# Kernel tuning notes

Hardware: AMD Instinct MI355X
Metric: run time of the kernel (lower is better)

Reference implementation:

```python
import jax, jax.numpy as jnp
import numpy as np

B, N, K, D = 256, 64, 12, 128


def setup_inputs() -> dict:
    key = jax.random.key(0)
    ks = jax.random.split(key, 12)
    s = 1.0 / np.sqrt(D)
    inp = {
        "nodes_hidden": jax.random.normal(ks[0], (B, N, D), jnp.float32),
        "neighbors_hidden": jax.random.normal(ks[1], (B, N, K, D), jnp.float32),
        # binary neighbor-validity mask (float, as in the torch code)
        "mask": (jax.random.uniform(ks[2], (B, N, K)) < 0.7).astype(jnp.float32),
        "Wq": jax.random.uniform(ks[3], (D, D), jnp.float32, -s, s),
        "bq": jax.random.uniform(ks[4], (D,), jnp.float32, -s, s),
        "Wk": jax.random.uniform(ks[5], (D, D), jnp.float32, -s, s),
        "bk": jax.random.uniform(ks[6], (D,), jnp.float32, -s, s),
        "Wv": jax.random.uniform(ks[7], (D, D), jnp.float32, -s, s),
        "bv": jax.random.uniform(ks[8], (D,), jnp.float32, -s, s),
        # W_att: Linear(2D -> 1); split into the query half and key half of its weight
        "wa_q": jax.random.uniform(ks[9], (D,), jnp.float32, -s, s),
        "wa_k": jax.random.uniform(ks[10], (D,), jnp.float32, -s, s),
        "ba": jax.random.uniform(ks[11], (), jnp.float32, -s, s),
    }
    return inp


def reference(nodes_hidden, neighbors_hidden, mask, Wq, bq, Wk, bk, Wv, bv, wa_q, wa_k, ba):
    # prepend the node itself to its neighbor list: [B,N,K+1,D]
    nh = jnp.concatenate([nodes_hidden[:, :, None, :], neighbors_hidden], axis=2)
    # prepend an always-valid slot to the mask: [B,N,K+1]
    m = jnp.concatenate([jnp.ones(mask.shape[:-1] + (1,), mask.dtype), mask], axis=-1)

    q = nodes_hidden @ Wq + bq            # [B,N,D]
    k = nh @ Wk + bk                      # [B,N,K+1,D]
    v = nh @ Wv + bv                      # [B,N,K+1,D]

    # W_att(cat([q,k])) == q.wa_q + k.wa_k + ba  (avoids materializing the 2D concat)
    sim = (q @ wa_q)[:, :, None] + k @ wa_k + ba   # [B,N,K+1]
    sim = jnp.where(sim >= 0, sim, 0.2 * sim)      # LeakyReLU(0.2)
    sim = jnp.exp(sim) * m                         # masked exp (matches torch exactly)
    attn = sim / (jnp.sum(sim, axis=-1, keepdims=True) + 1e-16)
    return jnp.einsum('bnk,bnkd->bnd', attn, v)    # [B,N,D]
```

## Files before the change

### kernel.cpp

```cpp
#include <hip/hip_runtime.h>


#define B_  256
#define N_  64
#define K_  12
#define D_  128
#define BN  (B_ * N_)
#define TP    4
#define TILES 4
#define ROWS  16
#define HB_STRIDE 132

__global__ void prep_kernel(const float* __restrict__ Wq, const float* __restrict__ bq,
                            const float* __restrict__ Wk, const float* __restrict__ bk,
                            const float* __restrict__ wa_q, const float* __restrict__ wa_k,
                            float* __restrict__ ws) {
    int g = blockIdx.x;
    int l = threadIdx.x;
    const float* row;
    const float* wa;
    float* outp;
    if (g < 128)      { row = Wq + g * D_;         wa = wa_q; outp = ws + g; }
    else if (g < 256) { row = Wk + (g - 128) * D_; wa = wa_k; outp = ws + 128 + (g - 128); }
    else if (g == 256){ row = bq;                  wa = wa_q; outp = ws + 256; }
    else              { row = bk;                  wa = wa_k; outp = ws + 257; }

    float2 r = ((const float2*)row)[l];
    float2 w = ((const float2*)wa)[l];
    float p = r.x * w.x + r.y * w.y;
    #pragma unroll
    for (int m = 1; m < 64; m <<= 1) p += __shfl_xor(p, m, 64);
    if (l == 0) *outp = p;
}

__device__ __forceinline__ void gll16(const float* g, float* l) {
    __builtin_amdgcn_global_load_lds(
        (const __attribute__((address_space(1))) unsigned int*)g,
        (__attribute__((address_space(3))) unsigned int*)l, 16, 0, 0);
}

__global__ void __launch_bounds__(256)
fused_kernel(const float* __restrict__ nodes, const float* __restrict__ neigh,
             const float* __restrict__ mask, const float* __restrict__ ba_p,
             const float* __restrict__ ws, const float* __restrict__ Wv,
             const float* __restrict__ bv, float* __restrict__ out) {
    __shared__ float nb[2][TP * K_ * D_];
    __shared__ float ndb[2][TP * D_];
    __shared__ float mb[2][TP * K_];
    __shared__ float hb[ROWS * HB_STRIDE];
    __shared__ float scL[ROWS];

    const int t    = threadIdx.x;
    const int wave = t >> 6;
    const int l    = t & 63;
    const int li   = l & 31;
    const int h    = l >> 5;
    const int j8   = l & 7;

    const float cq  = ws[256];
    const float ckb = ws[257];
    const float ba  = ba_p[0];
    const float cst = cq + ckb + ba;
    const float4 wqe4 = ((const float4*)ws)[li];
    const float4 wke4 = ((const float4*)(ws + 128))[li];

    const int base_pair = blockIdx.x * ROWS;

    #define STAGE(buf, tt) do {                                               \
        const int tb_ = base_pair + (tt) * TP;                                \
        const float* ns_ = neigh + (size_t)tb_ * (K_ * D_);                   \
        _Pragma("unroll")                                                     \
        for (int i_ = 0; i_ < 6; ++i_)                                        \
            gll16(ns_ + i_ * 1024 + t * 4, &nb[buf][i_ * 1024 + t * 4]);      \
        if (wave < 2)                                                         \
            gll16(nodes + (size_t)tb_ * D_ + t * 4, &ndb[buf][t * 4]);        \
        else if (wave == 2 && l < 12)                                         \
            gll16(mask + (size_t)tb_ * K_ + l * 4, &mb[buf][l * 4]);          \
    } while (0)

    #define COMPUTE(buf, tt) do {                                             \
        const float* nbp_ = &nb[buf][wave * (K_ * D_)];                       \
        const float* ndp_ = &ndb[buf][wave * D_];                             \
        const float4 nv_ = *(const float4*)(ndp_ + 4 * li);                   \
        float4 x0_ = *(const float4*)(nbp_ + (0 + h) * D_ + 4 * li);          \
        float4 x1_ = *(const float4*)(nbp_ + (2 + h) * D_ + 4 * li);          \
        float4 x2_ = *(const float4*)(nbp_ + (4 + h) * D_ + 4 * li);          \
        float4 x3_ = *(const float4*)(nbp_ + (6 + h) * D_ + 4 * li);          \
        float4 x4_ = *(const float4*)(nbp_ + (8 + h) * D_ + 4 * li);          \
        float4 x5_ = *(const float4*)(nbp_ + (10 + h) * D_ + 4 * li);         \
        float v0 = x0_.x*wke4.x + x0_.y*wke4.y + x0_.z*wke4.z + x0_.w*wke4.w; \
        float v1 = x1_.x*wke4.x + x1_.y*wke4.y + x1_.z*wke4.z + x1_.w*wke4.w; \
        float v2 = x2_.x*wke4.x + x2_.y*wke4.y + x2_.z*wke4.z + x2_.w*wke4.w; \
        float v3 = x3_.x*wke4.x + x3_.y*wke4.y + x3_.z*wke4.z + x3_.w*wke4.w; \
        float v4 = x4_.x*wke4.x + x4_.y*wke4.y + x4_.z*wke4.z + x4_.w*wke4.w; \
        float v5 = x5_.x*wke4.x + x5_.y*wke4.y + x5_.z*wke4.z + x5_.w*wke4.w; \
        float v6 = nv_.x*wke4.x + nv_.y*wke4.y + nv_.z*wke4.z + nv_.w*wke4.w; \
        float v7 = nv_.x*wqe4.x + nv_.y*wqe4.y + nv_.z*wqe4.z + nv_.w*wqe4.w; \
        float A0, A1, A2, A3;                                                 \
        {                                                                     \
            const bool hi_ = (l & 1);                                         \
            float g0 = __shfl_xor(hi_ ? v0 : v1, 1, 64);                      \
            float g1 = __shfl_xor(hi_ ? v2 : v3, 1, 64);                      \
            float g2 = __shfl_xor(hi_ ? v4 : v5, 1, 64);                      \
            float g3 = __shfl_xor(hi_ ? v6 : v7, 1, 64);                      \
            A0 = (hi_ ? v1 : v0) + g0;                                        \
            A1 = (hi_ ? v3 : v2) + g1;                                        \
            A2 = (hi_ ? v5 : v4) + g2;                                        \
            A3 = (hi_ ? v7 : v6) + g3;                                        \
        }                                                                     \
        float B0, B1;                                                         \
        {                                                                     \
            const bool hi_ = (l & 2);                                         \
            float g0 = __shfl_xor(hi_ ? A0 : A1, 2, 64);                      \
            float g1 = __shfl_xor(hi_ ? A2 : A3, 2, 64);                      \
            B0 = (hi_ ? A1 : A0) + g0;                                        \
            B1 = (hi_ ? A3 : A2) + g1;                                        \
        }                                                                     \
        float c;                                                              \
        {                                                                     \
            const bool hi_ = (l & 4);                                         \
            float g = __shfl_xor(hi_ ? B0 : B1, 4, 64);                       \
            c = (hi_ ? B1 : B0) + g;                                          \
        }                                                                     \
        c += __shfl_xor(c, 8, 64);                                            \
        c += __shfl_xor(c, 16, 64);                                           \
        const float pq_  = __shfl(c, 7, 8);                                   \
        const float pkn_ = __shfl(c, 6, 8);                                   \
        const float base_ = pq_ + cst;                                        \
        float s0_ = base_ + pkn_;                                             \
        s0_ = (s0_ >= 0.0f) ? s0_ : 0.2f * s0_;                               \
        const float e0_ = __expf(s0_);                                        \
        float sj_ = base_ + c;                                                \
        sj_ = (sj_ >= 0.0f) ? sj_ : 0.2f * sj_;                               \
        float ej_ = 0.0f;                                                     \
        if (j8 < 6) ej_ = __expf(sj_) * mb[buf][wave * K_ + 2 * j8 + h];      \
        const float an_ = (h == 0) ? e0_ : 0.0f;                              \
        float ax = an_ * nv_.x, ay = an_ * nv_.y;                             \
        float az = an_ * nv_.z, aw = an_ * nv_.w;                             \
        float Se_ = 0.0f;                                                     \
        {                                                                     \
            float bi_;                                                        \
            bi_ = __shfl(ej_, 0, 8); Se_ += bi_;                              \
            ax += bi_*x0_.x; ay += bi_*x0_.y; az += bi_*x0_.z; aw += bi_*x0_.w; \
            bi_ = __shfl(ej_, 1, 8); Se_ += bi_;                              \
            ax += bi_*x1_.x; ay += bi_*x1_.y; az += bi_*x1_.z; aw += bi_*x1_.w; \
            bi_ = __shfl(ej_, 2, 8); Se_ += bi_;                              \
            ax += bi_*x2_.x; ay += bi_*x2_.y; az += bi_*x2_.z; aw += bi_*x2_.w; \
            bi_ = __shfl(ej_, 3, 8); Se_ += bi_;                              \
            ax += bi_*x3_.x; ay += bi_*x3_.y; az += bi_*x3_.z; aw += bi_*x3_.w; \
            bi_ = __shfl(ej_, 4, 8); Se_ += bi_;                              \
            ax += bi_*x4_.x; ay += bi_*x4_.y; az += bi_*x4_.z; aw += bi_*x4_.w; \
            bi_ = __shfl(ej_, 5, 8); Se_ += bi_;                              \
            ax += bi_*x5_.x; ay += bi_*x5_.y; az += bi_*x5_.z; aw += bi_*x5_.w; \
        }                                                                     \
        ax += __shfl_xor(ax, 32, 64);                                         \
        ay += __shfl_xor(ay, 32, 64);                                         \
        az += __shfl_xor(az, 32, 64);                                         \
        aw += __shfl_xor(aw, 32, 64);                                         \
        Se_ += __shfl_xor(Se_, 32, 64);                                       \
        const float S_   = e0_ + Se_;                                         \
        const float inv_ = 1.0f / (S_ + 1e-16f);                              \
        if (h == 0) {                                                         \
            const int lrow_ = (tt) * TP + wave;                               \
            float4 o_;                                                        \
            o_.x = ax * inv_;                                                 \
            o_.y = ay * inv_;                                                 \
            o_.z = az * inv_;                                                 \
            o_.w = aw * inv_;                                                 \
            *(float4*)(hb + lrow_ * HB_STRIDE + 4 * li) = o_;                 \
            if (li == 0) scL[lrow_] = S_ * inv_;                              \
        }                                                                     \
    } while (0)

    STAGE(0, 0);
    __syncthreads();
    #pragma unroll
    for (int tt = 0; tt < TILES; ++tt) {
        const int cur = tt & 1;
        if (tt + 1 < TILES) STAGE((tt + 1) & 1, tt + 1);
        __builtin_amdgcn_sched_barrier(0);
        COMPUTE(cur, tt);
        __syncthreads();
    }
    #undef STAGE
    #undef COMPUTE

    const int rg = t >> 5;
    const int cg = t & 31;
    const float4* wv4 = (const float4*)Wv;
    const float* hr0 = hb + rg * HB_STRIDE;
    const float* hr1 = hb + (rg + 8) * HB_STRIDE;

    float4 acc0 = make_float4(0.0f, 0.0f, 0.0f, 0.0f);
    float4 acc1 = make_float4(0.0f, 0.0f, 0.0f, 0.0f);
    #pragma unroll 8
    for (int kq = 0; kq < 32; ++kq) {
        const float4 a0 = *(const float4*)(hr0 + 4 * kq);
        const float4 a1 = *(const float4*)(hr1 + 4 * kq);
        #pragma unroll
        for (int e = 0; e < 4; ++e) {
            const float4 w = wv4[(4 * kq + e) * 32 + cg];
            const float f0 = (e == 0) ? a0.x : (e == 1) ? a0.y : (e == 2) ? a0.z : a0.w;
            const float f1 = (e == 0) ? a1.x : (e == 1) ? a1.y : (e == 2) ? a1.z : a1.w;
            acc0.x += f0 * w.x; acc0.y += f0 * w.y;
            acc0.z += f0 * w.z; acc0.w += f0 * w.w;
            acc1.x += f1 * w.x; acc1.y += f1 * w.y;
            acc1.z += f1 * w.z; acc1.w += f1 * w.w;
        }
    }

    const float4 bvv = ((const float4*)bv)[cg];
    {
        const float s = scL[rg];
        float4 o;
        o.x = acc0.x + bvv.x * s;
        o.y = acc0.y + bvv.y * s;
        o.z = acc0.z + bvv.z * s;
        o.w = acc0.w + bvv.w * s;
        *(float4*)(out + (size_t)(base_pair + rg) * D_ + cg * 4) = o;
    }
    {
        const float s = scL[rg + 8];
        float4 o;
        o.x = acc1.x + bvv.x * s;
        o.y = acc1.y + bvv.y * s;
        o.z = acc1.z + bvv.z * s;
        o.w = acc1.w + bvv.w * s;
        *(float4*)(out + (size_t)(base_pair + rg + 8) * D_ + cg * 4) = o;
    }
}

extern "C" void kernel_launch(void* const* d_in, const int* in_sizes, int n_in,
                              void* d_out, int out_size, void* d_ws, size_t ws_size,
                              hipStream_t stream) {
    const float* nodes = (const float*)d_in[0];
    const float* neigh = (const float*)d_in[1];
    const float* mask  = (const float*)d_in[2];
    const float* Wq    = (const float*)d_in[3];
    const float* bq    = (const float*)d_in[4];
    const float* Wk    = (const float*)d_in[5];
    const float* bk    = (const float*)d_in[6];
    const float* Wv    = (const float*)d_in[7];
    const float* bv    = (const float*)d_in[8];
    const float* wa_q  = (const float*)d_in[9];
    const float* wa_k  = (const float*)d_in[10];
    const float* ba    = (const float*)d_in[11];
    float* out = (float*)d_out;
    float* ws  = (float*)d_ws;

    prep_kernel<<<258, 64, 0, stream>>>(Wq, bq, Wk, bk, wa_q, wa_k, ws);
    fused_kernel<<<BN / ROWS, 256, 0, stream>>>(nodes, neigh, mask, ba, ws, Wv, bv, out);
}
```

Before: 191.6 us.

## Give each wave private LDS slabs with vmcnt-based pipelining instead of block barriers

Each wave now stages and processes its own four consecutive node rows in two private LDS slots. It waits on its own outstanding global-to-LDS loads with s_waitcnt vmcnt rather than a block-wide __syncthreads per tile. Mask values are loaded straight into registers up front instead of being staged through LDS. This removes barrier stalls between waves and lets each wave overlap its next load with its current compute. In exchange, correctness now depends on hand-counted vmcnt values and on the in-order completion of these loads.

```diff
diff --git a/kernel.cpp b/kernel.cpp
--- a/kernel.cpp
+++ b/kernel.cpp
@@ -6,10 +6,9 @@
 #define K_  12
 #define D_  128
 #define BN  (B_ * N_)
-#define TP    4
-#define TILES 4
-#define ROWS  16
+#define ROWS 16
 #define HB_STRIDE 132
+#define SLOT_F 1664
 
 __global__ void prep_kernel(const float* __restrict__ Wq, const float* __restrict__ bq,
                             const float* __restrict__ Wk, const float* __restrict__ bk,
@@ -44,9 +43,7 @@
              const float* __restrict__ mask, const float* __restrict__ ba_p,
              const float* __restrict__ ws, const float* __restrict__ Wv,
              const float* __restrict__ bv, float* __restrict__ out) {
-    __shared__ float nb[2][TP * K_ * D_];
-    __shared__ float ndb[2][TP * D_];
-    __shared__ float mb[2][TP * K_];
+    __shared__ float slab[8][SLOT_F];
     __shared__ float hb[ROWS * HB_STRIDE];
     __shared__ float scL[ROWS];
 
@@ -65,29 +62,33 @@
     const float4 wke4 = ((const float4*)(ws + 128))[li];
 
     const int base_pair = blockIdx.x * ROWS;
-
-    #define STAGE(buf, tt) do {                                               \
-        const int tb_ = base_pair + (tt) * TP;                                \
-        const float* ns_ = neigh + (size_t)tb_ * (K_ * D_);                   \
+    const int idx0 = base_pair + wave * 4;
+
+    float mv0 = (j8 < 6) ? mask[(size_t)(idx0 + 0) * K_ + 2 * j8 + h] : 0.0f;
+    float mv1 = (j8 < 6) ? mask[(size_t)(idx0 + 1) * K_ + 2 * j8 + h] : 0.0f;
+    float mv2 = (j8 < 6) ? mask[(size_t)(idx0 + 2) * K_ + 2 * j8 + h] : 0.0f;
+    float mv3 = (j8 < 6) ? mask[(size_t)(idx0 + 3) * K_ + 2 * j8 + h] : 0.0f;
+
+    #define STAGE(p) do {                                                     \
+        const int idx_ = idx0 + (p);                                          \
+        float* sb_ = &slab[wave * 2 + ((p) & 1)][0];                          \
+        const float* ns_ = neigh + (size_t)idx_ * (K_ * D_);                  \
         _Pragma("unroll")                                                     \
         for (int i_ = 0; i_ < 6; ++i_)                                        \
-            gll16(ns_ + i_ * 1024 + t * 4, &nb[buf][i_ * 1024 + t * 4]);      \
-        if (wave < 2)                                                         \
-            gll16(nodes + (size_t)tb_ * D_ + t * 4, &ndb[buf][t * 4]);        \
-        else if (wave == 2 && l < 12)                                         \
-            gll16(mask + (size_t)tb_ * K_ + l * 4, &mb[buf][l * 4]);          \
+            gll16(ns_ + i_ * 256 + l * 4, sb_ + i_ * 256 + l * 4);            \
+        if (l < 32)                                                           \
+            gll16(nodes + (size_t)idx_ * D_ + l * 4, sb_ + 1536 + l * 4);     \
     } while (0)
 
-    #define COMPUTE(buf, tt) do {                                             \
-        const float* nbp_ = &nb[buf][wave * (K_ * D_)];                       \
-        const float* ndp_ = &ndb[buf][wave * D_];                             \
-        const float4 nv_ = *(const float4*)(ndp_ + 4 * li);                   \
-        float4 x0_ = *(const float4*)(nbp_ + (0 + h) * D_ + 4 * li);          \
-        float4 x1_ = *(const float4*)(nbp_ + (2 + h) * D_ + 4 * li);          \
-        float4 x2_ = *(const float4*)(nbp_ + (4 + h) * D_ + 4 * li);          \
-        float4 x3_ = *(const float4*)(nbp_ + (6 + h) * D_ + 4 * li);          \
-        float4 x4_ = *(const float4*)(nbp_ + (8 + h) * D_ + 4 * li);          \
-        float4 x5_ = *(const float4*)(nbp_ + (10 + h) * D_ + 4 * li);         \
+    #define COMPUTE(p, MV) do {                                               \
+        const float* sb_ = &slab[wave * 2 + ((p) & 1)][0];                    \
+        const float4 nv_ = *(const float4*)(sb_ + 1536 + 4 * li);             \
+        float4 x0_ = *(const float4*)(sb_ + (0 + h) * 128 + 4 * li);          \
+        float4 x1_ = *(const float4*)(sb_ + (2 + h) * 128 + 4 * li);          \
+        float4 x2_ = *(const float4*)(sb_ + (4 + h) * 128 + 4 * li);          \
+        float4 x3_ = *(const float4*)(sb_ + (6 + h) * 128 + 4 * li);          \
+        float4 x4_ = *(const float4*)(sb_ + (8 + h) * 128 + 4 * li);          \
+        float4 x5_ = *(const float4*)(sb_ + (10 + h) * 128 + 4 * li);         \
         float v0 = x0_.x*wke4.x + x0_.y*wke4.y + x0_.z*wke4.z + x0_.w*wke4.w; \
         float v1 = x1_.x*wke4.x + x1_.y*wke4.y + x1_.z*wke4.z + x1_.w*wke4.w; \
         float v2 = x2_.x*wke4.x + x2_.y*wke4.y + x2_.z*wke4.z + x2_.w*wke4.w; \
@@ -132,8 +133,7 @@
         const float e0_ = __expf(s0_);                                        \
         float sj_ = base_ + c;                                                \
         sj_ = (sj_ >= 0.0f) ? sj_ : 0.2f * sj_;                               \
-        float ej_ = 0.0f;                                                     \
-        if (j8 < 6) ej_ = __expf(sj_) * mb[buf][wave * K_ + 2 * j8 + h];      \
+        const float ej_ = __expf(sj_) * (MV);             \
         const float an_ = (h == 0) ? e0_ : 0.0f;                              \
         float ax = an_ * nv_.x, ay = an_ * nv_.y;                             \
         float az = an_ * nv_.z, aw = an_ * nv_.w;                             \
@@ -161,7 +161,7 @@
         const float S_   = e0_ + Se_;                                         \
         const float inv_ = 1.0f / (S_ + 1e-16f);                              \
         if (h == 0) {                                                         \
-            const int lrow_ = (tt) * TP + wave;                               \
+            const int lrow_ = wave * 4 + (p);                                 \
             float4 o_;                                                        \
             o_.x = ax * inv_;                                                 \
             o_.y = ay * inv_;                                                 \
@@ -172,18 +172,31 @@
         }                                                                     \
     } while (0)
 
-    STAGE(0, 0);
-    __syncthreads();
-    #pragma unroll
-    for (int tt = 0; tt < TILES; ++tt) {
-        const int cur = tt & 1;
-        if (tt + 1 < TILES) STAGE((tt + 1) & 1, tt + 1);
-        __builtin_amdgcn_sched_barrier(0);
-        COMPUTE(cur, tt);
-        __syncthreads();
-    }
+    #define VWAIT(n) do {                                                     \
+        asm volatile("s_waitcnt vmcnt(%0)" :: "i"(n) : "memory");             \
+        __builtin_amdgcn_sched_barrier(0);                                    \
+    } while (0)
+
+    STAGE(0);
+    __builtin_amdgcn_sched_barrier(0);
+    STAGE(1);
+    VWAIT(7);
+    COMPUTE(0, mv0);
+    __builtin_amdgcn_sched_barrier(0);
+    STAGE(2);
+    VWAIT(7);
+    COMPUTE(1, mv1);
+    __builtin_amdgcn_sched_barrier(0);
+    STAGE(3);
+    VWAIT(7);
+    COMPUTE(2, mv2);
+    __builtin_amdgcn_sched_barrier(0);
+    VWAIT(0);
+    COMPUTE(3, mv3);
     #undef STAGE
     #undef COMPUTE
+    #undef VWAIT
+    __syncthreads();
 
     const int rg = t >> 5;
     const int cg = t & 31;
```

Result: no change. 192.0 us (+0.2%).
